# Optimization experiments

Hardware: AMD Instinct MI355X
Metric: run time of the kernel (lower is better)

Reference implementation:

```python
import jax, jax.numpy as jnp
import numpy as np

B, L, HID, NH = 4, 1024, 768, 12
HD = HID // NH  # head dim 64
VOCAB, MPE = 30, 2048
NW, WL = 8, 16
BETA = 1.0


def setup_inputs() -> dict:
    key = jax.random.key(0)
    ks = jax.random.split(key, 10)
    hidden_states = jax.random.normal(ks[0], (B, L, HID), dtype=jnp.float32)
    attention_mask = jnp.zeros((B, 1, 1, L), dtype=jnp.float32)
    distance = jax.random.randint(ks[1], (B, L, L), 0, 1022, dtype=jnp.int32)
    random_walk = jax.random.randint(ks[2], (B, L, NW, WL), 0, VOCAB, dtype=jnp.int32)
    anonymous_random_walk = jax.random.randint(ks[3], (B, L, NW, WL), 0, VOCAB, dtype=jnp.int32)
    s = 0.02
    Wq = jax.random.normal(ks[4], (HID, HID), dtype=jnp.float32) * s
    Wk = jax.random.normal(ks[5], (HID, HID), dtype=jnp.float32) * s
    Wv = jax.random.normal(ks[6], (HID, HID), dtype=jnp.float32) * s
    bq = jnp.zeros((HID,), jnp.float32)
    bk = jnp.zeros((HID,), jnp.float32)
    bv = jnp.zeros((HID,), jnp.float32)
    node_emb = jax.random.normal(ks[7], (VOCAB, HID), dtype=jnp.float32) * s
    node_emb = node_emb.at[0].set(0.0)  # padding_idx=0
    dist_emb = jax.random.normal(ks[8], (MPE, NH), dtype=jnp.float32) * s
    dist_emb = dist_emb.at[0].set(0.0)  # padding_idx=0
    return dict(hidden_states=hidden_states, attention_mask=attention_mask,
                Wq=Wq, bq=bq, Wk=Wk, bk=bk, Wv=Wv, bv=bv,
                node_emb=node_emb, dist_emb=dist_emb,
                distance=distance, random_walk=random_walk,
                anonymous_random_walk=anonymous_random_walk)


def _heads(x):  # [B,L,HID] -> [B,NH,L,HD]
    return x.reshape(B, L, NH, HD).transpose(0, 2, 1, 3)


def _walk_bias(walk, node_emb):
    # walk: [B,L,NW,WL] int -> embed [B,L,NW,WL,HID] -> sum dims (2,3) -> [B,L,HID]
    pe = jnp.sum(node_emb[walk], axis=(2, 3))
    e = _heads(pe)  # [B,NH,L,HD]
    return jnp.einsum('bhid,bhjd->bhij', e, e)


def reference(hidden_states, attention_mask, Wq, bq, Wk, bk, Wv, bv,
              node_emb, dist_emb, distance, random_walk, anonymous_random_walk):
    q = _heads(hidden_states @ Wq.T + bq)
    k = _heads(hidden_states @ Wk.T + bk)
    v = _heads(hidden_states @ Wv.T + bv)
    scores = jnp.einsum('bhid,bhjd->bhij', q, k) / np.sqrt(HD).astype(np.float32)
    # distance RPE: [B,L,L,NH] -> [B,NH,L,L]
    bias = dist_emb[distance + 1].transpose(0, 3, 1, 2)
    bias = bias + _walk_bias(random_walk, node_emb)
    bias = bias + _walk_bias(anonymous_random_walk, node_emb)
    scores = scores + bias * BETA + attention_mask
    probs = jax.nn.softmax(scores, axis=-1)
    ctx = jnp.einsum('bhij,bhjd->bhid', probs, v)
    return ctx.transpose(0, 2, 1, 3).reshape(B, L, HID)
```

## Files before the change

### kernel.cpp

```cpp
#include <hip/hip_runtime.h>
#include <hip/hip_bf16.h>

#define LL 1024
#define HID 768
#define NH 12
#define HD 64
#define KAUG 192
#define NBH 48

typedef unsigned int u32;
typedef unsigned short u16;
typedef __bf16 bf16_t;
typedef bf16_t bf16x8 __attribute__((ext_vector_type(8)));
typedef _Float16 f16x4 __attribute__((ext_vector_type(4)));
typedef float f32x4 __attribute__((ext_vector_type(4)));
typedef u32 u32x4 __attribute__((ext_vector_type(4)));

__device__ __forceinline__ u16 f2b(float f) {
    union { float f; u32 u; } v; v.f = f;
    u32 r = v.u + 0x7fffu + ((v.u >> 16) & 1u);
    return (u16)(r >> 16);
}
__device__ __forceinline__ u16 f2h(float f) {
    _Float16 h = (_Float16)f;
    return __builtin_bit_cast(u16, h);
}
__device__ __forceinline__ bf16x8 load8s(const u16* p) {
    return __builtin_bit_cast(bf16x8, *reinterpret_cast<const u32x4*>(p));
}
__device__ __forceinline__ f16x4 load4h(const u16* p) {
    return __builtin_bit_cast(f16x4, *reinterpret_cast<const unsigned long long*>(p));
}
__device__ __forceinline__ void cvt4_store_v(u16* dst, float4 f) {
    ushort4 o;
    o.x = f2b(f.x); o.y = f2b(f.y); o.z = f2b(f.z); o.w = f2b(f.w);
    *reinterpret_cast<ushort4*>(dst) = o;
}

__global__ __launch_bounds__(256) void k_pre(const float* __restrict__ hs,
                                             const float* __restrict__ Wq, const float* __restrict__ Wk,
                                             const float* __restrict__ Wv,
                                             u16* __restrict__ hs16, u16* __restrict__ w16) {
    int bx = blockIdx.x;
    const float* src; u16* dst; int base;
    if (bx < 1536) { src = hs; dst = hs16; base = bx; }
    else {
        int w = bx - 1536;
        int which = w / 288;
        src = (which == 0) ? Wq : (which == 1) ? Wk : Wv;
        dst = w16 + (size_t)which * 768 * 768;
        base = w - which * 288;
    }
    int idx = (base * 256 + threadIdx.x) * 8;
    float4 a = *reinterpret_cast<const float4*>(&src[idx]);
    float4 b = *reinterpret_cast<const float4*>(&src[idx + 4]);
    cvt4_store_v(&dst[idx], a);
    cvt4_store_v(&dst[idx + 4], b);
}

__global__ __launch_bounds__(256) void k_qkvpe(const u16* __restrict__ hs16,
                                               const u16* __restrict__ w16,
                                               const float* __restrict__ bq, const float* __restrict__ bk,
                                               const float* __restrict__ bv,
                                               const int* __restrict__ rw, const int* __restrict__ arw,
                                               const float* __restrict__ node_emb,
                                               const int* __restrict__ distance,
                                               u16* __restrict__ Qa, u16* __restrict__ Ka,
                                               u16* __restrict__ Vt, u16* __restrict__ distu) {
    __shared__ __align__(16) u16 smem[18432];
    int lin = blockIdx.x;
    int tid = threadIdx.x;
    if (lin < 576) {
        u16* a_s = smem;
        u16* b_s = smem + 9216;
        int xcd = lin & 7, idx = lin >> 3;
        int mt = xcd * 4 + (idx & 3);
        int nt = idx >> 2;
        int m0 = mt * 128;
        int which = nt / 6;
        int n0w = (nt % 6) * 128;
        const u16* W = w16 + (size_t)which * 768 * 768;
        const float* bias = (which == 0) ? bq : (which == 1) ? bk : bv;
        int wave = tid >> 6, lane = tid & 63, l15 = lane & 15, qd = lane >> 4;
        int wm = wave >> 1, wn = wave & 1;
        int srow = tid >> 3, scol = (tid & 7) * 8;

        f32x4 acc[4][4];
        for (int i = 0; i < 4; i++)
            for (int j = 0; j < 4; j++) acc[i][j] = f32x4{0.f, 0.f, 0.f, 0.f};

        u32x4 pa[4], pb[4];
#pragma unroll
        for (int it = 0; it < 4; it++) {
            int row = srow + it * 32;
            pa[it] = *reinterpret_cast<const u32x4*>(&hs16[(size_t)(m0 + row) * 768 + scol]);
            pb[it] = *reinterpret_cast<const u32x4*>(&W[(size_t)(n0w + row) * 768 + scol]);
        }
        for (int k0 = 0; k0 < 768; k0 += 64) {
            __syncthreads();
#pragma unroll
            for (int it = 0; it < 4; it++) {
                int row = srow + it * 32;
                *reinterpret_cast<u32x4*>(&a_s[row * 72 + scol]) = pa[it];
                *reinterpret_cast<u32x4*>(&b_s[row * 72 + scol]) = pb[it];
            }
            __syncthreads();
            if (k0 < 704) {
                int k1 = k0 + 64;
#pragma unroll
                for (int it = 0; it < 4; it++) {
                    int row = srow + it * 32;
                    pa[it] = *reinterpret_cast<const u32x4*>(&hs16[(size_t)(m0 + row) * 768 + k1 + scol]);
                    pb[it] = *reinterpret_cast<const u32x4*>(&W[(size_t)(n0w + row) * 768 + k1 + scol]);
                }
            }
            for (int kk = 0; kk < 2; kk++) {
                bf16x8 af[4], bf[4];
                for (int i = 0; i < 4; i++) af[i] = load8s(&a_s[(wm * 64 + i * 16 + l15) * 72 + kk * 32 + qd * 8]);
                for (int j = 0; j < 4; j++) bf[j] = load8s(&b_s[(wn * 64 + j * 16 + l15) * 72 + kk * 32 + qd * 8]);
                for (int i = 0; i < 4; i++)
                    for (int j = 0; j < 4; j++)
                        acc[i][j] = __builtin_amdgcn_mfma_f32_16x16x32_bf16(af[i], bf[j], acc[i][j], 0, 0, 0);
            }
        }
        __syncthreads();
        int b = m0 >> 10, l0b = m0 & 1023;
        if (which != 2) {
            float qscale = (which == 0) ? 0.125f : 1.0f;
            for (int i = 0; i < 4; i++) {
                int m_loc = wm * 64 + i * 16 + qd * 4;
                for (int j = 0; j < 4; j++) {
                    int n_loc = wn * 64 + j * 16 + l15;
                    float bv_ = bias[n0w + n_loc];
                    for (int r = 0; r < 4; r++)
                        smem[(m_loc + r) * 136 + n_loc] = f2b((acc[i][j][r] + bv_) * qscale);
                }
            }
            __syncthreads();
            u16* dstbuf = (which == 0) ? Qa : Ka;
            for (int it = 0; it < 8; it++) {
                int c = tid + it * 256;
                int row = c >> 4, col = (c & 15) * 8;
                u32x4 w = *reinterpret_cast<u32x4*>(&smem[row * 136 + col]);
                int nn = n0w + col;
                int h = nn >> 6, d = nn & 63;
                size_t dst = ((size_t)(b * NH + h) * LL + (l0b + row)) * KAUG + d;
                *reinterpret_cast<u32x4*>(&dstbuf[dst]) = w;
            }
        } else {
            for (int i = 0; i < 4; i++) {
                int m_loc = wm * 64 + i * 16 + qd * 4;
                for (int j = 0; j < 4; j++) {
                    int n_loc = wn * 64 + j * 16 + l15;
                    float bv_ = bias[n0w + n_loc];
                    for (int r = 0; r < 4; r++)
                        smem[n_loc * 136 + (m_loc + r)] = f2h(acc[i][j][r] + bv_);
                }
            }
            __syncthreads();
            for (int it = 0; it < 8; it++) {
                int c = tid + it * 256;
                int n = c >> 4, m_off = (c & 15) * 8;
                u32x4 w = *reinterpret_cast<u32x4*>(&smem[n * 136 + m_off]);
                int nn = n0w + n;
                int h = nn >> 6, d = nn & 63;
                size_t dst = ((size_t)(b * NH + h) * HD + d) * LL + (l0b + m_off);
                *reinterpret_cast<u32x4*>(&Vt[dst]) = w;
            }
        }
    } else if (lin < 4672) {
        int m = lin - 576;
        int* hist = (int*)smem;
        float* c1 = (float*)(smem + 128);
        float* c2 = (float*)(smem + 192);
        u16* pe_s = smem + 256;
        int t = tid;
        if (t < 64) hist[t] = 0;
        __syncthreads();
        if (t < 128) atomicAdd(&hist[rw[m * 128 + t] & 31], 1);
        else         atomicAdd(&hist[32 + (arw[m * 128 + (t - 128)] & 31)], 1);
        __syncthreads();
        if (t < 64) {
            if (t < 32) c1[t] = (float)hist[t];
            else        c2[t - 32] = (float)hist[t];
        }
        __syncthreads();
        for (int c = t; c < 768; c += 256) {
            float s1 = 0.f, s2 = 0.f;
            for (int v = 0; v < 30; v++) {
                float ne = node_emb[v * 768 + c];
                s1 += c1[v] * ne;
                s2 += c2[v] * ne;
            }
            int h = c >> 6, d = c & 63;
            pe_s[h * 128 + d]      = f2b(s1);
            pe_s[h * 128 + 64 + d] = f2b(s2);
        }
        __syncthreads();
        int b = m >> 10, l = m & 1023;
        if (t < 192) {
            int h = t >> 4, ch = t & 15;
            u32x4 w = *reinterpret_cast<const u32x4*>(&pe_s[h * 128 + ch * 8]);
            size_t dst = ((size_t)(b * NH + h) * LL + l) * KAUG + 64 + ch * 8;
            *reinterpret_cast<u32x4*>(&Qa[dst]) = w;
            *reinterpret_cast<u32x4*>(&Ka[dst]) = w;
        }
    } else {
        int idx = ((lin - 4672) * 256 + tid) * 8;
        int4 a = *reinterpret_cast<const int4*>(&distance[idx]);
        int4 b = *reinterpret_cast<const int4*>(&distance[idx + 4]);
        u32x4 w;
        w[0] = (u32)(u16)(a.x + 1) | ((u32)(u16)(a.y + 1) << 16);
        w[1] = (u32)(u16)(a.z + 1) | ((u32)(u16)(a.w + 1) << 16);
        w[2] = (u32)(u16)(b.x + 1) | ((u32)(u16)(b.y + 1) << 16);
        w[3] = (u32)(u16)(b.z + 1) | ((u32)(u16)(b.w + 1) << 16);
        *reinterpret_cast<u32x4*>(&distu[idx]) = w;
    }
}

__global__ __launch_bounds__(256, 2) void k_attn(const u16* __restrict__ Qa, const u16* __restrict__ Ka,
                                                 const u16* __restrict__ Vt,
                                                 const u16* __restrict__ distu,
                                                 const float* __restrict__ dist_emb,
                                                 const float* __restrict__ mask,
                                                 void* __restrict__ outv, int f32mode) {
    __shared__ __align__(16) u16 ka_s[64][200];
    __shared__ __align__(16) u16 vt_s[64][80];
    __shared__ float distcol[2048];

    int lin = blockIdx.x + (blockIdx.y << 4);
    int xcd = lin & 7, slot = lin >> 3;
    int bh = xcd * 6 + (slot >> 4);
    int itile = slot & 15;
    int b = bh / NH, h = bh % NH;
    int tid = threadIdx.x, wave = tid >> 6, lane = tid & 63, l15 = lane & 15, qd = lane >> 4;

    const u16* Qh = Qa + (size_t)bh * LL * KAUG;
    const u16* Kh = Ka + (size_t)bh * LL * KAUG;
    const u16* Vh = Vt + (size_t)bh * HD * LL;
    const u16* distb = distu + (size_t)b * LL * LL;
    const float* maskb = mask + (size_t)b * LL;

    for (int t = tid; t < 2048; t += 256) distcol[t] = dist_emb[t * NH + h];

    int i0 = itile * 64 + wave * 16;
    bf16x8 aq[6];
#pragma unroll
    for (int ks = 0; ks < 6; ks++)
        aq[ks] = load8s(&Qh[(size_t)(i0 + l15) * KAUG + ks * 32 + qd * 8]);

    f32x4 o[4];
#pragma unroll
    for (int i = 0; i < 4; i++) o[i] = f32x4{0.f, 0.f, 0.f, 0.f};
    float m_i = -1e30f, l_i = 0.f;

    u32x4 kbuf[6], vbuf[2];
    ushort4 dp[4];
#pragma unroll
    for (int it = 0; it < 6; it++) {
        int c = tid + it * 256;
        int row = c / 24, col = (c % 24) * 8;
        kbuf[it] = *reinterpret_cast<const u32x4*>(&Kh[(size_t)row * KAUG + col]);
    }
#pragma unroll
    for (int it = 0; it < 2; it++) {
        int c = tid + it * 256;
        int d = c >> 3, col = (c & 7) * 8;
        vbuf[it] = *reinterpret_cast<const u32x4*>(&Vh[(size_t)d * LL + col]);
    }
#pragma unroll
    for (int jf = 0; jf < 4; jf++)
        dp[jf] = *reinterpret_cast<const ushort4*>(&distb[(size_t)(i0 + l15) * LL + jf * 16 + qd * 4]);

    for (int jt = 0; jt < 16; jt++) {
        int j0 = jt * 64;
        __syncthreads();
#pragma unroll
        for (int it = 0; it < 6; it++) {
            int c = tid + it * 256;
            int row = c / 24, col = (c % 24) * 8;
            *reinterpret_cast<u32x4*>(&ka_s[row][col]) = kbuf[it];
        }
#pragma unroll
        for (int it = 0; it < 2; it++) {
            int c = tid + it * 256;
            int d = c >> 3, col = (c & 7) * 8;
            *reinterpret_cast<u32x4*>(&vt_s[d][col]) = vbuf[it];
        }
        __syncthreads();
        if (jt < 15) {
            int j0n = j0 + 64;
#pragma unroll
            for (int it = 0; it < 6; it++) {
                int c = tid + it * 256;
                int row = c / 24, col = (c % 24) * 8;
                kbuf[it] = *reinterpret_cast<const u32x4*>(&Kh[(size_t)(j0n + row) * KAUG + col]);
            }
#pragma unroll
            for (int it = 0; it < 2; it++) {
                int c = tid + it * 256;
                int d = c >> 3, col = (c & 7) * 8;
                vbuf[it] = *reinterpret_cast<const u32x4*>(&Vh[(size_t)d * LL + j0n + col]);
            }
        }

        f32x4 st[4];
#pragma unroll
        for (int jf = 0; jf < 4; jf++) st[jf] = f32x4{0.f, 0.f, 0.f, 0.f};
        __builtin_amdgcn_s_setprio(1);
#pragma unroll
        for (int ks = 0; ks < 6; ks++) {
#pragma unroll
            for (int jf = 0; jf < 4; jf++) {
                bf16x8 ak = load8s(&ka_s[jf * 16 + l15][ks * 32 + qd * 8]);
                st[jf] = __builtin_amdgcn_mfma_f32_16x16x32_bf16(ak, aq[ks], st[jf], 0, 0, 0);
            }
        }
        __builtin_amdgcn_s_setprio(0);
#pragma unroll
        for (int jf = 0; jf < 4; jf++) {
            float4 mk = *reinterpret_cast<const float4*>(&maskb[j0 + jf * 16 + qd * 4]);
            st[jf][0] += distcol[dp[jf].x] + mk.x;
            st[jf][1] += distcol[dp[jf].y] + mk.y;
            st[jf][2] += distcol[dp[jf].z] + mk.z;
            st[jf][3] += distcol[dp[jf].w] + mk.w;
        }
        if (jt < 15) {
            int j0n = j0 + 64;
#pragma unroll
            for (int jf = 0; jf < 4; jf++)
                dp[jf] = *reinterpret_cast<const ushort4*>(&distb[(size_t)(i0 + l15) * LL + j0n + jf * 16 + qd * 4]);
        }

        float m0_ = fmaxf(fmaxf(st[0][0], st[0][1]), fmaxf(st[0][2], st[0][3]));
        float m1_ = fmaxf(fmaxf(st[1][0], st[1][1]), fmaxf(st[1][2], st[1][3]));
        float m2_ = fmaxf(fmaxf(st[2][0], st[2][1]), fmaxf(st[2][2], st[2][3]));
        float m3_ = fmaxf(fmaxf(st[3][0], st[3][1]), fmaxf(st[3][2], st[3][3]));
        float mx = fmaxf(fmaxf(m0_, m1_), fmaxf(m2_, m3_));
        mx = fmaxf(mx, __shfl_xor(mx, 16));
        mx = fmaxf(mx, __shfl_xor(mx, 32));
        if (!__all(mx <= m_i + 8.0f)) {
            float mnew = fmaxf(m_i, mx);
            float alpha = __expf(m_i - mnew);
            m_i = mnew;
            l_i *= alpha;
            float a0 = __shfl(alpha, qd * 4 + 0, 16);
            float a1 = __shfl(alpha, qd * 4 + 1, 16);
            float a2 = __shfl(alpha, qd * 4 + 2, 16);
            float a3 = __shfl(alpha, qd * 4 + 3, 16);
#pragma unroll
            for (int df = 0; df < 4; df++) {
                o[df][0] *= a0; o[df][1] *= a1; o[df][2] *= a2; o[df][3] *= a3;
            }
        }
        float ssum = 0.f;
        f16x4 pf[4];
#pragma unroll
        for (int jf = 0; jf < 4; jf++) {
            float p0 = __expf(st[jf][0] - m_i);
            float p1 = __expf(st[jf][1] - m_i);
            float p2 = __expf(st[jf][2] - m_i);
            float p3 = __expf(st[jf][3] - m_i);
            ssum += (p0 + p1) + (p2 + p3);
            pf[jf] = f16x4{(_Float16)p0, (_Float16)p1, (_Float16)p2, (_Float16)p3};
        }
        ssum += __shfl_xor(ssum, 16);
        ssum += __shfl_xor(ssum, 32);
        l_i += ssum;
        __builtin_amdgcn_s_setprio(1);
#pragma unroll
        for (int jf = 0; jf < 4; jf++) {
#pragma unroll
            for (int df = 0; df < 4; df++) {
                f16x4 vf = load4h(&vt_s[df * 16 + l15][jf * 16 + qd * 4]);
                o[df] = __builtin_amdgcn_mfma_f32_16x16x16f16(pf[jf], vf, o[df], 0, 0, 0);
            }
        }
        __builtin_amdgcn_s_setprio(0);
    }

    float lr0 = 1.f / __shfl(l_i, qd * 4 + 0, 16);
    float lr1 = 1.f / __shfl(l_i, qd * 4 + 1, 16);
    float lr2 = 1.f / __shfl(l_i, qd * 4 + 2, 16);
    float lr3 = 1.f / __shfl(l_i, qd * 4 + 3, 16);
#pragma unroll
    for (int df = 0; df < 4; df++) {
        int d = df * 16 + l15;
        float v0 = o[df][0] * lr0, v1 = o[df][1] * lr1, v2 = o[df][2] * lr2, v3 = o[df][3] * lr3;
        int i_abs = i0 + qd * 4;
        size_t idx = ((size_t)(b * LL) + i_abs) * HID + h * 64 + d;
        if (f32mode) {
            float* op = (float*)outv;
            op[idx] = v0; op[idx + HID] = v1; op[idx + 2 * HID] = v2; op[idx + 3 * HID] = v3;
        } else {
            u16* op = (u16*)outv;
            op[idx] = f2b(v0); op[idx + HID] = f2b(v1); op[idx + 2 * HID] = f2b(v2); op[idx + 3 * HID] = f2b(v3);
        }
    }
}

extern "C" void kernel_launch(void* const* d_in, const int* in_sizes, int n_in,
                              void* d_out, int out_size, void* d_ws, size_t ws_size,
                              hipStream_t stream) {
    const float* hs       = (const float*)d_in[0];
    const float* mask     = (const float*)d_in[1];
    const float* Wq       = (const float*)d_in[2];
    const float* bq       = (const float*)d_in[3];
    const float* Wk       = (const float*)d_in[4];
    const float* bk       = (const float*)d_in[5];
    const float* Wv       = (const float*)d_in[6];
    const float* bv       = (const float*)d_in[7];
    const float* node_emb = (const float*)d_in[8];
    const float* dist_emb = (const float*)d_in[9];
    const int* distance   = (const int*)d_in[10];
    const int* rw         = (const int*)d_in[11];
    const int* arw        = (const int*)d_in[12];

    int f32mode = 0;
    {
        hipDeviceptr_t base = nullptr; size_t sz = 0;
        if (hipMemGetAddressRange(&base, &sz, (hipDeviceptr_t)d_out) == hipSuccess) {
            size_t off = (size_t)((char*)d_out - (char*)base);
            if (sz - off >= (size_t)out_size * 4u) f32mode = 1;
        }
    }

    u16* Qa = (u16*)d_ws;
    u16* Ka = Qa + (size_t)NBH * LL * KAUG;
    u16* Vt = Ka + (size_t)NBH * LL * KAUG;
    u16* distu = Vt + (size_t)NBH * HD * LL;
    u16* hs16 = distu + (size_t)4 * LL * LL;
    u16* w16  = hs16 + (size_t)4096 * 768;

    k_pre<<<dim3(2400), dim3(256), 0, stream>>>(hs, Wq, Wk, Wv, hs16, w16);
    k_qkvpe<<<dim3(6720), dim3(256), 0, stream>>>(hs16, w16, bq, bk, bv, rw, arw, node_emb,
                                                  distance, Qa, Ka, Vt, distu);
    k_attn<<<dim3(16, 48), dim3(256), 0, stream>>>(Qa, Ka, Vt, distu, dist_emb, mask, d_out, f32mode);
}
```

Before: 214.9 us.

## Double-buffer K/V shared-memory tiles to use one barrier per iteration

```diff
diff --git a/kernel.cpp b/kernel.cpp
--- a/kernel.cpp
+++ b/kernel.cpp
@@ -224,8 +224,8 @@
                                                  const float* __restrict__ dist_emb,
                                                  const float* __restrict__ mask,
                                                  void* __restrict__ outv, int f32mode) {
-    __shared__ __align__(16) u16 ka_s[64][200];
-    __shared__ __align__(16) u16 vt_s[64][80];
+    __shared__ __align__(16) u16 ka_s[2][64][200];
+    __shared__ __align__(16) u16 vt_s[2][64][80];
     __shared__ float distcol[2048];
 
     int lin = blockIdx.x + (blockIdx.y << 4);
@@ -256,53 +256,46 @@
 
     u32x4 kbuf[6], vbuf[2];
     ushort4 dp[4];
-#pragma unroll
-    for (int it = 0; it < 6; it++) {
-        int c = tid + it * 256;
-        int row = c / 24, col = (c % 24) * 8;
-        kbuf[it] = *reinterpret_cast<const u32x4*>(&Kh[(size_t)row * KAUG + col]);
-    }
-#pragma unroll
-    for (int it = 0; it < 2; it++) {
-        int c = tid + it * 256;
-        int d = c >> 3, col = (c & 7) * 8;
-        vbuf[it] = *reinterpret_cast<const u32x4*>(&Vh[(size_t)d * LL + col]);
-    }
-#pragma unroll
-    for (int jf = 0; jf < 4; jf++)
-        dp[jf] = *reinterpret_cast<const ushort4*>(&distb[(size_t)(i0 + l15) * LL + jf * 16 + qd * 4]);
-
-    for (int jt = 0; jt < 16; jt++) {
-        int j0 = jt * 64;
-        __syncthreads();
+    auto loadKV = [&](int j0) {
 #pragma unroll
         for (int it = 0; it < 6; it++) {
             int c = tid + it * 256;
             int row = c / 24, col = (c % 24) * 8;
-            *reinterpret_cast<u32x4*>(&ka_s[row][col]) = kbuf[it];
+            kbuf[it] = *reinterpret_cast<const u32x4*>(&Kh[(size_t)(j0 + row) * KAUG + col]);
         }
 #pragma unroll
         for (int it = 0; it < 2; it++) {
             int c = tid + it * 256;
             int d = c >> 3, col = (c & 7) * 8;
-            *reinterpret_cast<u32x4*>(&vt_s[d][col]) = vbuf[it];
-        }
-        __syncthreads();
-        if (jt < 15) {
-            int j0n = j0 + 64;
-#pragma unroll
-            for (int it = 0; it < 6; it++) {
-                int c = tid + it * 256;
-                int row = c / 24, col = (c % 24) * 8;
-                kbuf[it] = *reinterpret_cast<const u32x4*>(&Kh[(size_t)(j0n + row) * KAUG + col]);
-            }
-#pragma unroll
-            for (int it = 0; it < 2; it++) {
-                int c = tid + it * 256;
-                int d = c >> 3, col = (c & 7) * 8;
-                vbuf[it] = *reinterpret_cast<const u32x4*>(&Vh[(size_t)d * LL + j0n + col]);
-            }
-        }
+            vbuf[it] = *reinterpret_cast<const u32x4*>(&Vh[(size_t)d * LL + j0 + col]);
+        }
+    };
+    auto dumpKV = [&](int buf) {
+#pragma unroll
+        for (int it = 0; it < 6; it++) {
+            int c = tid + it * 256;
+            int row = c / 24, col = (c % 24) * 8;
+            *reinterpret_cast<u32x4*>(&ka_s[buf][row][col]) = kbuf[it];
+        }
+#pragma unroll
+        for (int it = 0; it < 2; it++) {
+            int c = tid + it * 256;
+            int d = c >> 3, col = (c & 7) * 8;
+            *reinterpret_cast<u32x4*>(&vt_s[buf][d][col]) = vbuf[it];
+        }
+    };
+
+    loadKV(0);
+#pragma unroll
+    for (int jf = 0; jf < 4; jf++)
+        dp[jf] = *reinterpret_cast<const ushort4*>(&distb[(size_t)(i0 + l15) * LL + jf * 16 + qd * 4]);
+    dumpKV(0);
+    __syncthreads();
+
+    for (int jt = 0; jt < 16; jt++) {
+        int j0 = jt * 64;
+        int cur = jt & 1;
+        if (jt < 15) loadKV(j0 + 64);
 
         f32x4 st[4];
 #pragma unroll
@@ -312,7 +305,7 @@
         for (int ks = 0; ks < 6; ks++) {
 #pragma unroll
             for (int jf = 0; jf < 4; jf++) {
-                bf16x8 ak = load8s(&ka_s[jf * 16 + l15][ks * 32 + qd * 8]);
+                bf16x8 ak = load8s(&ka_s[cur][jf * 16 + l15][ks * 32 + qd * 8]);
                 st[jf] = __builtin_amdgcn_mfma_f32_16x16x32_bf16(ak, aq[ks], st[jf], 0, 0, 0);
             }
         }
@@ -372,11 +365,16 @@
         for (int jf = 0; jf < 4; jf++) {
 #pragma unroll
             for (int df = 0; df < 4; df++) {
-                f16x4 vf = load4h(&vt_s[df * 16 + l15][jf * 16 + qd * 4]);
+                f16x4 vf = load4h(&vt_s[cur][df * 16 + l15][jf * 16 + qd * 4]);
                 o[df] = __builtin_amdgcn_mfma_f32_16x16x16f16(pf[jf], vf, o[df], 0, 0, 0);
             }
         }
         __builtin_amdgcn_s_setprio(0);
+
+        if (jt < 15) {
+            dumpKV(cur ^ 1);
+            __syncthreads();
+        }
     }
 
     float lr0 = 1.f / __shfl(l_i, qd * 4 + 0, 16);
```

Measured after the change: 220.3 us. +2.5%, slower.
